# Performance work log

Measured on AMD Instinct MI355X. Metric: run time of the kernel, lower is better.

The kernel has to match this reference:

```python
import jax, jax.numpy as jnp
import numpy as np

NUM_HEADS = 8
NUM_LEVELS = 4
NUM_POINTS = 16
NUM_BEV = 2
EMBED = 256
BS = 64
NQ = NUM_LEVELS * NUM_POINTS  # 64


def _bilinear_sample(img, grid):
    """F.grid_sample(mode='bilinear', padding_mode='zeros', align_corners=False).
    img: (N, C, H, W); grid: (N, Hg, Wg, 2) in [-1, 1] (x, y). Returns (N, C, Hg, Wg)."""
    N, C, H, W = img.shape
    gx = (grid[..., 0] + 1.0) * (W * 0.5) - 0.5  # (N, Hg, Wg)
    gy = (grid[..., 1] + 1.0) * (H * 0.5) - 0.5
    x0 = jnp.floor(gx)
    y0 = jnp.floor(gy)
    flat = img.reshape(N, C, H * W)

    def gather(xi, yi):
        valid = (xi >= 0) & (xi <= W - 1) & (yi >= 0) & (yi <= H - 1)
        xc = jnp.clip(xi, 0, W - 1).astype(jnp.int32)
        yc = jnp.clip(yi, 0, H - 1).astype(jnp.int32)
        idx = (yc * W + xc).reshape(N, 1, -1)
        g = jnp.take_along_axis(flat, idx, axis=2).reshape(N, C, xi.shape[1], xi.shape[2])
        return g * valid[:, None, :, :].astype(img.dtype)

    wx1 = (gx - x0)[:, None]  # (N,1,Hg,Wg)
    wy1 = (gy - y0)[:, None]
    v00 = gather(x0, y0)
    v01 = gather(x0 + 1.0, y0)
    v10 = gather(x0, y0 + 1.0)
    v11 = gather(x0 + 1.0, y0 + 1.0)
    top = v00 * (1.0 - wx1) + v01 * wx1
    bot = v10 * (1.0 - wx1) + v11 * wx1
    return top * (1.0 - wy1) + bot * wy1


def _forward(query, key_hist, value_hist, reference_points, W_off, b_off, spatial_shapes):
    bs, nq, d = query.shape
    Hn, L, P, BEV = NUM_HEADS, NUM_LEVELS, NUM_POINTS, NUM_BEV
    dh = d // Hn
    Pb = P * BEV
    ss = np.asarray(spatial_shapes)  # (L, 2) static (h, w)

    queries = jnp.concatenate([query, query], axis=1)           # (bs, 2*nq, d)
    keies = jnp.concatenate([query, key_hist], axis=1)
    values = jnp.concatenate([query, value_hist], axis=1)
    qb = queries.shape[1]

    # sampling offsets projection (the only used learned linear in the original forward)
    off = (queries @ W_off + b_off).reshape(bs, qb, Hn, Pb, L, 2)

    # NOTE: original re-assigns q/k/v from the RAW concatenated tensors (to_Q/to_K/to_V discarded)
    qh = queries.reshape(bs, qb, Hn, dh)
    kh = keies.reshape(bs, qb, Hn, dh)
    vh = values.reshape(bs, qb, Hn, dh)

    attn = jax.nn.softmax(jnp.einsum('bqhd,bkhd->bqhk', qh, kh), axis=-1)
    attn = attn.reshape(bs, qb, Hn, L, Pb)

    rp = jnp.concatenate([reference_points, reference_points], axis=1)  # (bs, qb, L, 2)
    norm = jnp.stack([jnp.asarray(ss[:, 1], jnp.float32),
                      jnp.asarray(ss[:, 0], jnp.float32)], axis=-1)      # (L, 2) = (w, h)
    loc = rp[:, :, None, None, :, :] + off / norm                        # (bs,qb,H,Pb,L,2)
    # FAITHFUL: original uses .view here (pure reshape, not a transpose)
    loc = loc.reshape(bs, qb, Hn, L, Pb, 2)
    grids = 2.0 * loc - 1.0

    sampled = []
    start = 0
    for l in range(L):
        h_, w_ = int(ss[l, 0]), int(ss[l, 1])
        vl = vh[:, start:start + h_ * w_]                                # (bs, hw, H, dh)
        start += h_ * w_
        img = vl.transpose(0, 2, 3, 1).reshape(bs * Hn, dh, h_, w_)      # (bs*H, dh, h, w)
        grid_l = grids[:, :, :, l].transpose(0, 2, 1, 3, 4).reshape(bs * Hn, qb, Pb, 2)
        sampled.append(_bilinear_sample(img, grid_l))                    # (bs*H, dh, qb, Pb)

    samp = jnp.stack(sampled, axis=-2).reshape(bs * Hn, dh, qb, L * Pb)
    aw = attn.transpose(0, 2, 1, 3, 4).reshape(bs * Hn, 1, qb, L * Pb)
    out = (samp * aw).sum(-1)                                            # (bs*H, dh, qb)
    # FAITHFUL: original reshapes q_bev dim as (nq, BEV) and means over BEV
    out = out.reshape(bs, Hn * dh, nq, BEV).mean(-1).transpose(0, 2, 1)  # (bs, nq, d)
    return out + query  # dropout is identity at eval


def setup_inputs() -> dict:
    key = jax.random.key(0)
    ks = jax.random.split(key, 6)
    query = jax.random.normal(ks[0], (BS, NQ, EMBED), jnp.float32)
    key_hist = jax.random.normal(ks[1], (BS, NQ, EMBED), jnp.float32)
    value_hist = jax.random.normal(ks[2], (BS, NQ, EMBED), jnp.float32)
    reference_points = jax.random.uniform(ks[3], (BS, NQ, NUM_LEVELS, 2), jnp.float32)
    spatial_shapes = jnp.array([[4, 8]] * NUM_LEVELS, dtype=jnp.int32)  # sum(h*w)=128=L*P*BEV
    off_dim = NUM_HEADS * NUM_BEV * NUM_POINTS * NUM_LEVELS * 2
    W_off = jax.random.normal(ks[4], (EMBED, off_dim), jnp.float32) * 0.02
    b_off = jnp.zeros((off_dim,), jnp.float32)
    return {"query": query, "key_hist": key_hist, "value_hist": value_hist,
            "reference_points": reference_points, "spatial_shapes": spatial_shapes,
            "W_off": W_off, "b_off": b_off}


def reference(query, key_hist, value_hist, reference_points, spatial_shapes, W_off, b_off):
    return _forward(query, key_hist, value_hist, reference_points, W_off, b_off, spatial_shapes)
```

## Files before the change

kernel.cpp:

```cpp
#include <hip/hip_runtime.h>


typedef short  s16x8 __attribute__((ext_vector_type(8)));
typedef short  s16x4 __attribute__((ext_vector_type(4)));
typedef float  f32x4 __attribute__((ext_vector_type(4)));

__device__ __forceinline__ unsigned short f2bf(float f) {
    union { float f; unsigned u; } v; v.f = f;
    unsigned r = v.u + 0x7FFFu + ((v.u >> 16) & 1u);
    return (unsigned short)(r >> 16);
}
__device__ __forceinline__ float bf2f(unsigned short u) {
    return __uint_as_float(((unsigned)u) << 16);
}

__global__ __launch_bounds__(256) void prep(
    const float* __restrict__ W, const float* __restrict__ query,
    const float* __restrict__ key_hist, const float* __restrict__ value_hist,
    short* __restrict__ Wtb, short* __restrict__ Qb, short* __restrict__ Khb,
    short* __restrict__ VTg)
{
    __shared__ float s[32][33];
    const int bx = blockIdx.x, t = threadIdx.x;
    if (bx < 512) {
        const int n0 = (bx & 63) * 32, k0 = (bx >> 6) * 32;
        const int c = t & 31, r0 = t >> 5;
        #pragma unroll
        for (int p = 0; p < 4; ++p) {
            const int r = r0 + p * 8;
            s[r][c] = W[(size_t)(k0 + r) * 2048 + n0 + c];
        }
        __syncthreads();
        #pragma unroll
        for (int p = 0; p < 4; ++p) {
            const int r = r0 + p * 8;
            Wtb[(size_t)(n0 + r) * 256 + k0 + c] = (short)f2bf(s[c][r]);
        }
    } else if (bx < 2560) {
        const int j = bx - 512;
        const bool isK = j >= 1024;
        const float* src = isK ? key_hist : query;
        short* dst = isK ? Khb : Qb;
        const int i4 = ((j & 1023) * 256 + t) * 4;
        const float4 v = *(const float4*)(src + i4);
        s16x4 o;
        o.x = (short)f2bf(v.x); o.y = (short)f2bf(v.y);
        o.z = (short)f2bf(v.z); o.w = (short)f2bf(v.w);
        *(s16x4*)(dst + i4) = o;
    } else {
        const int bh = bx - 2560;
        const int b = bh >> 3, h = bh & 7;
        #pragma unroll
        for (int pass = 0; pass < 4; ++pass) {
            const int idx = t + 256 * pass;
            const int p = idx >> 3;
            const int dg = idx & 7;
            const float* src = (p < 64) ? query : value_hist;
            const float4 v = *(const float4*)(src +
                (size_t)(b * 64 + (p & 63)) * 256 + h * 32 + dg * 4);
            short* o = VTg + ((size_t)bh * 32 + dg * 4) * 128 + p;
            o[0 * 128] = (short)f2bf(v.x);
            o[1 * 128] = (short)f2bf(v.y);
            o[2 * 128] = (short)f2bf(v.z);
            o[3 * 128] = (short)f2bf(v.w);
        }
    }
}

__global__ __launch_bounds__(256) void gemm_k(
    const short* __restrict__ Ab, const short* __restrict__ Wt,
    const float* __restrict__ bias, short* __restrict__ OFFb)
{
    __shared__ __align__(16) short smem[128 * 136];
    short (*Asl)[40] = (short (*)[40])smem;
    short (*Bsl)[40] = (short (*)[40])(smem + 128 * 40);
    short (*Cst)[136] = (short (*)[136])smem;

    const int n0 = blockIdx.x * 128, m0 = blockIdx.y * 128;
    const int t = threadIdx.x, lane = t & 63, wave = t >> 6;
    const int wm0 = (wave >> 1) * 64, wn0 = (wave & 1) * 64;
    const int r = lane & 15, q = lane >> 4;

    f32x4 acc[4][4] = {};
    for (int kc = 0; kc < 256; kc += 32) {
        #pragma unroll
        for (int ss = 0; ss < 2; ++ss) {
            const int seg = t + ss * 256;
            const int row = seg >> 2, off8 = (seg & 3) * 8;
            *(s16x8*)&Asl[row][off8] =
                *(const s16x8*)(Ab + (size_t)(m0 + row) * 256 + kc + off8);
            *(s16x8*)&Bsl[row][off8] =
                *(const s16x8*)(Wt + (size_t)(n0 + row) * 256 + kc + off8);
        }
        __syncthreads();
        s16x8 af[4], bf[4];
        #pragma unroll
        for (int i = 0; i < 4; ++i) {
            af[i] = *(const s16x8*)&Asl[wm0 + i * 16 + r][q * 8];
            bf[i] = *(const s16x8*)&Bsl[wn0 + i * 16 + r][q * 8];
        }
        #pragma unroll
        for (int i = 0; i < 4; ++i)
            #pragma unroll
            for (int j = 0; j < 4; ++j)
                acc[i][j] = __builtin_amdgcn_mfma_f32_16x16x32_bf16(
                    af[i], bf[j], acc[i][j], 0, 0, 0);
        __syncthreads();
    }
    #pragma unroll
    for (int j = 0; j < 4; ++j) {
        const float bb = bias[n0 + wn0 + j * 16 + r];
        #pragma unroll
        for (int i = 0; i < 4; ++i)
            #pragma unroll
            for (int rg = 0; rg < 4; ++rg)
                Cst[wm0 + i * 16 + q * 4 + rg][wn0 + j * 16 + r] =
                    (short)f2bf(acc[i][j][rg] + bb);
    }
    __syncthreads();
    {
        const int row = t >> 1, half = t & 1;
        short* gdst = OFFb + (size_t)(m0 + row) * 2048 + n0 + half * 64;
        const short* lsrc = &Cst[row][half * 64];
        #pragma unroll
        for (int u = 0; u < 8; ++u)
            *(s16x8*)(gdst + u * 8) = *(const s16x8*)(lsrc + u * 8);
    }
}

__global__ __launch_bounds__(256) void scatter_av(
    const float* __restrict__ query, const float* __restrict__ refp,
    const short* __restrict__ Qb, const short* __restrict__ Khb,
    const short* __restrict__ VTg, const unsigned* __restrict__ OFFu,
    float* __restrict__ out)
{
    const int h = blockIdx.x, b = blockIdx.y, s = blockIdx.z;
    const int q0 = s * 32;
    const int t = threadIdx.x, lane = t & 63, wave = t >> 6;
    const int quad = lane >> 4, col = lane & 15;
    const int mw = wave & 1;

    __shared__ __align__(16) short attLb[32 * 136];
    __shared__ __align__(16) float Am[32 * 132];
    short* Amb = (short*)Am;

    {
        #pragma unroll
        for (int u = 0; u < 17; ++u) {
            const int idx = t + 256 * u;
            if (idx < 32 * 132) Am[idx] = 0.f;
        }
    }

    {
        const s16x8 aq = *(const s16x8*)(Qb +
            ((size_t)b * 64 + q0 + mw * 16 + col) * 256 + h * 32 + quad * 8);
        f32x4 lacc[8];
        #pragma unroll
        for (int t8 = 0; t8 < 8; ++t8) {
            const short* src = (t8 < 4)
                ? (Qb  + ((size_t)b * 64 + 16 * t8 + col) * 256)
                : (Khb + ((size_t)b * 64 + 16 * (t8 - 4) + col) * 256);
            const s16x8 bk = *(const s16x8*)(src + h * 32 + quad * 8);
            const f32x4 z = {0.f, 0.f, 0.f, 0.f};
            lacc[t8] = __builtin_amdgcn_mfma_f32_16x16x32_bf16(aq, bk, z, 0, 0, 0);
        }
        if (wave < 2) {
            #pragma unroll
            for (int r = 0; r < 4; ++r) {
                float m = lacc[0][r];
                #pragma unroll
                for (int t8 = 1; t8 < 8; ++t8) m = fmaxf(m, lacc[t8][r]);
                #pragma unroll
                for (int sh = 1; sh < 16; sh <<= 1) m = fmaxf(m, __shfl_xor(m, sh, 64));
                float e[8], ssum = 0.f;
                #pragma unroll
                for (int t8 = 0; t8 < 8; ++t8) {
                    e[t8] = __expf(lacc[t8][r] - m); ssum += e[t8];
                }
                #pragma unroll
                for (int sh = 1; sh < 16; sh <<= 1) ssum += __shfl_xor(ssum, sh, 64);
                const float inv = 1.0f / ssum;
                const int ql = mw * 16 + 4 * quad + r;
                #pragma unroll
                for (int t8 = 0; t8 < 8; ++t8)
                    attLb[ql * 136 + 16 * t8 + col] = (short)f2bf(e[t8] * inv);
            }
        }
    }
    __syncthreads();

    {
        const int q = t >> 3, fg = t & 7;
        const int qg = b * 64 + q0 + q;
        const unsigned* offrow = OFFu + (size_t)qg * 1024 + h * 128;
        const float* rp8 = refp + (size_t)qg * 8;
        float rpl[8];
        #pragma unroll
        for (int j = 0; j < 8; ++j) rpl[j] = rp8[j];
        float* rowW = &Am[q * 132];
        const short* arow = &attLb[q * 136];
        for (int i = 0; i < 16; ++i) {
            const int f = fg + 8 * i;
            const unsigned u = offrow[f];
            const float ox = __uint_as_float(u << 16);
            const float oy = __uint_as_float(u & 0xFFFF0000u);
            const float a = bf2f((unsigned short)arow[f]);
            const int l = f & 3;
            const float gx = 8.f * (rpl[l * 2 + 0] + ox * 0.125f) - 0.5f;
            const float gy = 4.f * (rpl[l * 2 + 1] + oy * 0.25f) - 0.5f;
            const float x0f = floorf(gx), y0f = floorf(gy);
            const float wx = gx - x0f, wy = gy - y0f;
            const int x0 = (int)x0f, y0 = (int)y0f;
            const int base = (f >> 5) * 32;
            const bool xv0 = (x0 >= 0) && (x0 < 8);
            const bool xv1 = (x0 >= -1) && (x0 < 7);
            const bool yv0 = (y0 >= 0) && (y0 < 4);
            const bool yv1 = (y0 >= -1) && (y0 < 3);
            if (xv0 && yv0) unsafeAtomicAdd(&rowW[base + y0 * 8 + x0],           a * (1.f - wx) * (1.f - wy));
            if (xv1 && yv0) unsafeAtomicAdd(&rowW[base + y0 * 8 + x0 + 1],       a * wx * (1.f - wy));
            if (xv0 && yv1) unsafeAtomicAdd(&rowW[base + (y0 + 1) * 8 + x0],     a * (1.f - wx) * wy);
            if (xv1 && yv1) unsafeAtomicAdd(&rowW[base + (y0 + 1) * 8 + x0 + 1], a * wx * wy);
        }
    }
    __syncthreads();

    {
        const int cq = t >> 3, cc = (t & 7) * 16;
        float vreg[16];
        #pragma unroll
        for (int u = 0; u < 4; ++u) {
            const float4 v = *(const float4*)&Am[cq * 132 + cc + 4 * u];
            vreg[4 * u + 0] = v.x; vreg[4 * u + 1] = v.y;
            vreg[4 * u + 2] = v.z; vreg[4 * u + 3] = v.w;
        }
        __syncthreads();
        #pragma unroll
        for (int u = 0; u < 2; ++u) {
            s16x8 o;
            #pragma unroll
            for (int j = 0; j < 8; ++j) o[j] = (short)f2bf(vreg[u * 8 + j]);
            *(s16x8*)&Amb[cq * 136 + cc + u * 8] = o;
        }
    }
    __syncthreads();

    {
        const int nt = wave >> 1;
        f32x4 oacc = {};
        #pragma unroll
        for (int ks = 0; ks < 4; ++ks) {
            const s16x8 af = *(const s16x8*)&Amb[(mw * 16 + col) * 136
                                                 + ks * 32 + quad * 8];
            const s16x8 bv = *(const s16x8*)(VTg +
                ((size_t)(b * 8 + h) * 32 + nt * 16 + col) * 128
                + ks * 32 + quad * 8);
            oacc = __builtin_amdgcn_mfma_f32_16x16x32_bf16(af, bv, oacc, 0, 0, 0);
        }
        const int d = h * 32 + nt * 16 + col;
        #pragma unroll
        for (int pr = 0; pr < 2; ++pr) {
            const float avg = 0.5f * (oacc[2 * pr] + oacc[2 * pr + 1]);
            const int pj = (q0 >> 1) + mw * 8 + quad * 2 + pr;
            const size_t re = ((size_t)b * 64 + pj) * 256 + d;
            const size_t ro = ((size_t)b * 64 + pj + 32) * 256 + d;
            out[re] = query[re] + avg;
            out[ro] = query[ro] + avg;
        }
    }
}

extern "C" void kernel_launch(void* const* d_in, const int* in_sizes, int n_in,
                              void* d_out, int out_size, void* d_ws, size_t ws_size,
                              hipStream_t stream) {
    (void)in_sizes; (void)n_in; (void)out_size; (void)ws_size;
    const float* query      = (const float*)d_in[0];
    const float* key_hist   = (const float*)d_in[1];
    const float* value_hist = (const float*)d_in[2];
    const float* refp       = (const float*)d_in[3];
    const float* W_off      = (const float*)d_in[5];
    const float* b_off      = (const float*)d_in[6];

    char* ws = (char*)d_ws;
    short* Qb   = (short*)(ws);
    short* Khb  = (short*)(ws + (2u << 20));
    short* Wtb  = (short*)(ws + (4u << 20));
    short* VTg  = (short*)(ws + (5u << 20));
    short* OFFb = (short*)(ws + (9u << 20));
    float* out  = (float*)d_out;

    prep<<<3072, 256, 0, stream>>>(W_off, query, key_hist, value_hist,
                                   Wtb, Qb, Khb, VTg);
    gemm_k<<<dim3(16, 32), 256, 0, stream>>>(Qb, Wtb, b_off, OFFb);
    scatter_av<<<dim3(8, 64, 2), 256, 0, stream>>>(query, refp, Qb, Khb, VTg,
                                                   (const unsigned*)OFFb, out);
}
```

Measured before the change: 176.0 us.

## Split attention logits/softmax into separate kernel and prefetch offsets into registers

Moves the QK logits and softmax out of scatter_av into a new logits_k kernel that reads fp32 query/key directly and converts to bf16 on the fly. This drops the key_hist bf16 conversion from prep and removes the duplicated logit computation that each z-slice block did before. scatter_av now loads offsets, attention weights and reference points into registers up front, overlapping these loads with the LDS zeroing, and fully unrolls the scatter loop. In exchange it adds a kernel launch and a global round trip for the attention matrix, and raises register use.

```diff
diff --git a/kernel.cpp b/kernel.cpp
--- a/kernel.cpp
+++ b/kernel.cpp
@@ -13,12 +13,19 @@
 __device__ __forceinline__ float bf2f(unsigned short u) {
     return __uint_as_float(((unsigned)u) << 16);
 }
+__device__ __forceinline__ s16x8 pack8(const float4 a, const float4 b) {
+    s16x8 o;
+    o[0] = (short)f2bf(a.x); o[1] = (short)f2bf(a.y);
+    o[2] = (short)f2bf(a.z); o[3] = (short)f2bf(a.w);
+    o[4] = (short)f2bf(b.x); o[5] = (short)f2bf(b.y);
+    o[6] = (short)f2bf(b.z); o[7] = (short)f2bf(b.w);
+    return o;
+}
 
 __global__ __launch_bounds__(256) void prep(
     const float* __restrict__ W, const float* __restrict__ query,
-    const float* __restrict__ key_hist, const float* __restrict__ value_hist,
-    short* __restrict__ Wtb, short* __restrict__ Qb, short* __restrict__ Khb,
-    short* __restrict__ VTg)
+    const float* __restrict__ value_hist,
+    short* __restrict__ Wtb, short* __restrict__ Qb, short* __restrict__ VTg)
 {
     __shared__ float s[32][33];
     const int bx = blockIdx.x, t = threadIdx.x;
@@ -36,19 +43,16 @@
             const int r = r0 + p * 8;
             Wtb[(size_t)(n0 + r) * 256 + k0 + c] = (short)f2bf(s[c][r]);
         }
-    } else if (bx < 2560) {
+    } else if (bx < 1536) {
         const int j = bx - 512;
-        const bool isK = j >= 1024;
-        const float* src = isK ? key_hist : query;
-        short* dst = isK ? Khb : Qb;
-        const int i4 = ((j & 1023) * 256 + t) * 4;
-        const float4 v = *(const float4*)(src + i4);
+        const int i4 = (j * 256 + t) * 4;
+        const float4 v = *(const float4*)(query + i4);
         s16x4 o;
         o.x = (short)f2bf(v.x); o.y = (short)f2bf(v.y);
         o.z = (short)f2bf(v.z); o.w = (short)f2bf(v.w);
-        *(s16x4*)(dst + i4) = o;
+        *(s16x4*)(Qb + i4) = o;
     } else {
-        const int bh = bx - 2560;
+        const int bh = bx - 1536;
         const int b = bh >> 3, h = bh & 7;
         #pragma unroll
         for (int pass = 0; pass < 4; ++pass) {
@@ -128,21 +132,85 @@
     }
 }
 
+__global__ __launch_bounds__(256) void logits_k(
+    const float* __restrict__ query, const float* __restrict__ key_hist,
+    short* __restrict__ attG)
+{
+    const int h = blockIdx.x, b = blockIdx.y;
+    const int t = threadIdx.x, lane = t & 63, wave = t >> 6;
+    const int quad = lane >> 4, col = lane & 15;
+
+    const float* qp = query + ((size_t)b * 64 + wave * 16 + col) * 256
+                      + h * 32 + quad * 8;
+    const s16x8 aq = pack8(*(const float4*)qp, *(const float4*)(qp + 4));
+    f32x4 lacc[8];
+    #pragma unroll
+    for (int t8 = 0; t8 < 8; ++t8) {
+        const float* kp = ((t8 < 4)
+            ? (query    + ((size_t)b * 64 + 16 * t8 + col) * 256)
+            : (key_hist + ((size_t)b * 64 + 16 * (t8 - 4) + col) * 256))
+            + h * 32 + quad * 8;
+        const s16x8 bk = pack8(*(const float4*)kp, *(const float4*)(kp + 4));
+        const f32x4 z = {0.f, 0.f, 0.f, 0.f};
+        lacc[t8] = __builtin_amdgcn_mfma_f32_16x16x32_bf16(aq, bk, z, 0, 0, 0);
+    }
+    #pragma unroll
+    for (int r = 0; r < 4; ++r) {
+        float m = lacc[0][r];
+        #pragma unroll
+        for (int t8 = 1; t8 < 8; ++t8) m = fmaxf(m, lacc[t8][r]);
+        #pragma unroll
+        for (int sh = 1; sh < 16; sh <<= 1) m = fmaxf(m, __shfl_xor(m, sh, 64));
+        float e[8], ssum = 0.f;
+        #pragma unroll
+        for (int t8 = 0; t8 < 8; ++t8) {
+            e[t8] = __expf(lacc[t8][r] - m); ssum += e[t8];
+        }
+        #pragma unroll
+        for (int sh = 1; sh < 16; sh <<= 1) ssum += __shfl_xor(ssum, sh, 64);
+        const float inv = 1.0f / ssum;
+        const int q = wave * 16 + 4 * quad + r;
+        short* dst = attG + ((size_t)(b * 8 + h) * 64 + q) * 128;
+        #pragma unroll
+        for (int t8 = 0; t8 < 8; ++t8)
+            dst[16 * t8 + col] = (short)f2bf(e[t8] * inv);
+    }
+}
+
 __global__ __launch_bounds__(256) void scatter_av(
     const float* __restrict__ query, const float* __restrict__ refp,
-    const short* __restrict__ Qb, const short* __restrict__ Khb,
     const short* __restrict__ VTg, const unsigned* __restrict__ OFFu,
-    float* __restrict__ out)
+    const short* __restrict__ attG, float* __restrict__ out)
 {
     const int h = blockIdx.x, b = blockIdx.y, s = blockIdx.z;
     const int q0 = s * 32;
     const int t = threadIdx.x, lane = t & 63, wave = t >> 6;
     const int quad = lane >> 4, col = lane & 15;
-    const int mw = wave & 1;
-
-    __shared__ __align__(16) short attLb[32 * 136];
+
     __shared__ __align__(16) float Am[32 * 132];
     short* Amb = (short*)Am;
+
+    const int q = t >> 3, fg = t & 7;
+    const int qg = b * 64 + q0 + q;
+    unsigned offv[16];
+    {
+        const unsigned* offrow = OFFu + (size_t)qg * 1024 + h * 128;
+        #pragma unroll
+        for (int i = 0; i < 16; ++i) offv[i] = offrow[fg + 8 * i];
+    }
+    float av[16];
+    {
+        const short* arow = attG + ((size_t)(b * 8 + h) * 64 + q0 + q) * 128;
+        #pragma unroll
+        for (int i = 0; i < 16; ++i)
+            av[i] = bf2f((unsigned short)arow[fg + 8 * i]);
+    }
+    float rpl[8];
+    {
+        const float* rp8 = refp + (size_t)qg * 8;
+        #pragma unroll
+        for (int j = 0; j < 8; ++j) rpl[j] = rp8[j];
+    }
 
     {
         #pragma unroll
@@ -151,61 +219,17 @@
             if (idx < 32 * 132) Am[idx] = 0.f;
         }
     }
-
-    {
-        const s16x8 aq = *(const s16x8*)(Qb +
-            ((size_t)b * 64 + q0 + mw * 16 + col) * 256 + h * 32 + quad * 8);
-        f32x4 lacc[8];
-        #pragma unroll
-        for (int t8 = 0; t8 < 8; ++t8) {
-            const short* src = (t8 < 4)
-                ? (Qb  + ((size_t)b * 64 + 16 * t8 + col) * 256)
-                : (Khb + ((size_t)b * 64 + 16 * (t8 - 4) + col) * 256);
-            const s16x8 bk = *(const s16x8*)(src + h * 32 + quad * 8);
-            const f32x4 z = {0.f, 0.f, 0.f, 0.f};
-            lacc[t8] = __builtin_amdgcn_mfma_f32_16x16x32_bf16(aq, bk, z, 0, 0, 0);
-        }
-        if (wave < 2) {
-            #pragma unroll
-            for (int r = 0; r < 4; ++r) {
-                float m = lacc[0][r];
-                #pragma unroll
-                for (int t8 = 1; t8 < 8; ++t8) m = fmaxf(m, lacc[t8][r]);
-                #pragma unroll
-                for (int sh = 1; sh < 16; sh <<= 1) m = fmaxf(m, __shfl_xor(m, sh, 64));
-                float e[8], ssum = 0.f;
-                #pragma unroll
-                for (int t8 = 0; t8 < 8; ++t8) {
-                    e[t8] = __expf(lacc[t8][r] - m); ssum += e[t8];
-                }
-                #pragma unroll
-                for (int sh = 1; sh < 16; sh <<= 1) ssum += __shfl_xor(ssum, sh, 64);
-                const float inv = 1.0f / ssum;
-                const int ql = mw * 16 + 4 * quad + r;
-                #pragma unroll
-                for (int t8 = 0; t8 < 8; ++t8)
-                    attLb[ql * 136 + 16 * t8 + col] = (short)f2bf(e[t8] * inv);
-            }
-        }
-    }
     __syncthreads();
 
     {
-        const int q = t >> 3, fg = t & 7;
-        const int qg = b * 64 + q0 + q;
-        const unsigned* offrow = OFFu + (size_t)qg * 1024 + h * 128;
-        const float* rp8 = refp + (size_t)qg * 8;
-        float rpl[8];
-        #pragma unroll
-        for (int j = 0; j < 8; ++j) rpl[j] = rp8[j];
         float* rowW = &Am[q * 132];
-        const short* arow = &attLb[q * 136];
+        #pragma unroll
         for (int i = 0; i < 16; ++i) {
             const int f = fg + 8 * i;
-            const unsigned u = offrow[f];
+            const unsigned u = offv[i];
             const float ox = __uint_as_float(u << 16);
             const float oy = __uint_as_float(u & 0xFFFF0000u);
-            const float a = bf2f((unsigned short)arow[f]);
+            const float a = av[i];
             const int l = f & 3;
             const float gx = 8.f * (rpl[l * 2 + 0] + ox * 0.125f) - 0.5f;
             const float gy = 4.f * (rpl[l * 2 + 1] + oy * 0.25f) - 0.5f;
@@ -246,7 +270,7 @@
     __syncthreads();
 
     {
-        const int nt = wave >> 1;
+        const int mw = wave & 1, nt = wave >> 1;
         f32x4 oacc = {};
         #pragma unroll
         for (int ks = 0; ks < 4; ++ks) {
@@ -283,15 +307,16 @@
 
     char* ws = (char*)d_ws;
     short* Qb   = (short*)(ws);
-    short* Khb  = (short*)(ws + (2u << 20));
-    short* Wtb  = (short*)(ws + (4u << 20));
-    short* VTg  = (short*)(ws + (5u << 20));
-    short* OFFb = (short*)(ws + (9u << 20));
+    short* Wtb  = (short*)(ws + (2u  << 20));
+    short* VTg  = (short*)(ws + (3u  << 20));
+    short* attG = (short*)(ws + (7u  << 20));
+    short* OFFb = (short*)(ws + (15u << 20));
     float* out  = (float*)d_out;
 
-    prep<<<3072, 256, 0, stream>>>(W_off, query, key_hist, value_hist,
-                                   Wtb, Qb, Khb, VTg);
+    prep<<<2048, 256, 0, stream>>>(W_off, query, value_hist, Wtb, Qb, VTg);
     gemm_k<<<dim3(16, 32), 256, 0, stream>>>(Qb, Wtb, b_off, OFFb);
-    scatter_av<<<dim3(8, 64, 2), 256, 0, stream>>>(query, refp, Qb, Khb, VTg,
-                                                   (const unsigned*)OFFb, out);
-}
+    logits_k<<<dim3(8, 64), 256, 0, stream>>>(query, key_hist, attG);
+    scatter_av<<<dim3(8, 64, 2), 256, 0, stream>>>(query, refp, VTg,
+                                                   (const unsigned*)OFFb,
+                                                   attG, out);
+}
```

Measured after the change: 177.2 us. Within noise of the previous version (+0.7%).
